# Kernel tuning notes

Hardware: AMD Instinct MI355X
Metric: run time of the kernel (lower is better)

Reference implementation:

```python
import jax, jax.numpy as jnp
import numpy as np

N_NODES = 50000
IN_CH = 128
HID = 256
N_EDGES = 500000


def setup_inputs() -> dict:
    key = jax.random.key(0)
    ks = jax.random.split(key, 16)
    glorot = lambda k, fi, fo: jax.random.normal(k, (fi, fo), jnp.float32) * (2.0 / (fi + fo)) ** 0.5
    return {
        "x": jax.random.normal(ks[0], (N_NODES, IN_CH), jnp.float32),
        "edge_index": jax.random.randint(ks[1], (2, N_EDGES), 0, N_NODES),
        "guidance_features": jax.random.normal(ks[2], (N_NODES, IN_CH), jnp.float32),
        "labels": jax.random.randint(ks[3], (N_NODES,), 0, 2),
        # state_encoder: Linear(3*in, hid) -> ReLU -> Linear(hid, hid)
        "se_w1": glorot(ks[4], IN_CH * 3, HID), "se_b1": jnp.zeros((HID,), jnp.float32),
        "se_w2": glorot(ks[5], HID, HID), "se_b2": jnp.zeros((HID,), jnp.float32),
        # policy_net: Linear(hid, hid//2) -> ReLU -> Linear(hid//2, 1) -> Sigmoid
        "pw1": glorot(ks[6], HID, HID // 2), "pb1": jnp.zeros((HID // 2,), jnp.float32),
        "pw2": glorot(ks[7], HID // 2, 1), "pb2": jnp.zeros((1,), jnp.float32),
        # value_predictor: Linear(hid, hid//2) -> ReLU -> Linear(hid//2, 1)
        "vw1": glorot(ks[8], HID, HID // 2), "vb1": jnp.zeros((HID // 2,), jnp.float32),
        "vw2": glorot(ks[9], HID // 2, 1), "vb2": jnp.zeros((1,), jnp.float32),
    }


def reference(x, edge_index, guidance_features, labels,
              se_w1, se_b1, se_w2, se_b2,
              pw1, pb1, pw2, pb2,
              vw1, vb1, vw2, vb2):
    row, col = edge_index[0], edge_index[1]
    # gather + concat -> [E, 3*in_ch]
    state = jnp.concatenate([x[row], x[col], guidance_features[col]], axis=1)
    # state_encoder
    h = jax.nn.relu(state @ se_w1 + se_b1) @ se_w2 + se_b2  # [E, hid]
    # policy_net (sigmoid)
    probs = jax.nn.sigmoid(jax.nn.relu(h @ pw1 + pb1) @ pw2 + pb2)  # [E, 1]
    # eval-mode actions (training=False branch)
    actions = (probs > 0.5).astype(jnp.float32)  # [E, 1]
    # value predictor + BCE-with-logits vs labels[row]
    z = jax.nn.relu(h @ vw1 + vb1) @ vw2 + vb2  # [E, 1]
    y = labels[row].astype(jnp.float32)[:, None]
    value_loss = jnp.mean(jnp.maximum(z, 0.0) - z * y + jnp.log1p(jnp.exp(-jnp.abs(z))))
    # NOTE: torch version also returns edge_index[:, actions>0] which has a
    # data-dependent shape; we return the dense action mask instead (jit-safe).
    return value_loss, actions
```

## Files before the change

### kernel.cpp

```cpp
#include <hip/hip_runtime.h>
#include <cstddef>

#define TE 56
#define NTHREADS 512

typedef float v2f __attribute__((ext_vector_type(2)));

#define PK_LO(accv, av, wv) \
  asm("v_pk_fma_f32 %0, %1, %2, %0 op_sel:[0,0,0] op_sel_hi:[0,1,1]" \
      : "+v"(accv) : "v"(av), "v"(wv))
#define PK_HI(accv, av, wv) \
  asm("v_pk_fma_f32 %0, %1, %2, %0 op_sel:[1,0,0] op_sel_hi:[1,1,1]" \
      : "+v"(accv) : "v"(av), "v"(wv))

#define SH_OFF    0
#define SW_OFF    14336
#define SW2_OFF   (SW_OFF + 4096)
#define SLOSS_OFF (SW2_OFF + 256)
#define SROW_OFF  (SLOSS_OFF + 64)
#define SCOL_OFF  (SROW_OFF + 64)
#define SMEM_FLOATS (SCOL_OFF + 64)

__device__ __forceinline__ void gld16(const float* g, float* l) {
  __builtin_amdgcn_global_load_lds(
      (const __attribute__((address_space(1))) void*)g,
      (__attribute__((address_space(3))) void*)l, 16, 0, 0);
}

__global__ __launch_bounds__(NTHREADS, 4)
void fused_edge_mlp(
    const float* __restrict__ x,
    const int*   __restrict__ edge_index,
    const float* __restrict__ gf,
    const int*   __restrict__ labels,
    const float* __restrict__ se_w1, const float* __restrict__ se_b1,
    const float* __restrict__ se_w2, const float* __restrict__ se_b2,
    const float* __restrict__ pw1,  const float* __restrict__ pb1,
    const float* __restrict__ pw2,  const float* __restrict__ pb2,
    const float* __restrict__ vw1,  const float* __restrict__ vb1,
    const float* __restrict__ vw2,  const float* __restrict__ vb2,
    float* __restrict__ out,
    float* __restrict__ ws_partial,
    int n_edges)
{
  extern __shared__ float smem[];
  float* sH    = smem + SH_OFF;
  float* sA    = smem + SH_OFF;
  float* sW    = smem + SW_OFF;
  float* sW2   = smem + SW2_OFF;
  float* sLoss = smem + SLOSS_OFF;
  int*   sRow  = (int*)(smem + SROW_OFF);
  int*   sCol  = (int*)(smem + SCOL_OFF);

  const int t  = threadIdx.x;
  const int e0 = blockIdx.x * TE;

  const int tc  = t & 31;
  const int teh = t >> 5;
  const int te  = teh & 7;
  const int ch  = teh >> 3;
  const int colBase = ch * 128 + tc * 4;

  const int wr  = t >> 6;
  const int wc4 = t & 63;

  if (t < TE) {
    int eg = e0 + t;
    sRow[t] = (eg < n_edges) ? edge_index[eg] : 0;
  } else if (t < 2 * TE) {
    int eg = e0 + (t - TE);
    sCol[t - TE] = (eg < n_edges) ? edge_index[(size_t)n_edges + eg] : 0;
  } else if (t >= 128 && t < 384) {
    int c = t - 128;
    sW2[c] = (c < 128) ? pw2[c] : vw2[c - 128];
  }

  v2f acc[7][2];
  auto zero_acc = [&]() {
    #pragma unroll
    for (int i = 0; i < 7; ++i) {
      acc[i][0] = v2f{0.f, 0.f};
      acc[i][1] = v2f{0.f, 0.f};
    }
  };

  auto issueW1 = [&](int c, int b) {
    gld16(&se_w1[((size_t)(c * 8 + wr)) * 256 + wc4 * 4], &sW[b * 2048 + t * 4]);
  };
  auto issueW2 = [&](int c, int b) {
    gld16(&se_w2[((size_t)(c * 8 + wr)) * 256 + wc4 * 4], &sW[b * 2048 + t * 4]);
  };
  auto issueW3 = [&](int c, int b) {
    int row = c * 8 + wr;
    const float* src = (wc4 < 32) ? &pw1[(size_t)row * 128 + wc4 * 4]
                                  : &vw1[(size_t)row * 128 + (wc4 - 32) * 4];
    gld16(src, &sW[b * 2048 + t * 4]);
  };

  auto stageA_issue = [&](int seg, int b) {
    const float* src = (seg == 2) ? gf : x;
    const int*   idx = (seg == 0) ? sRow : sCol;
    float* dst = sA + b * 7168;
    #pragma unroll
    for (int j = 0; j < 3; ++j) {
      int i4 = t + j * NTHREADS;
      int r = i4 >> 5, c4 = i4 & 31;
      gld16(&src[(size_t)idx[r] * 128 + c4 * 4], &dst[i4 * 4]);
    }
    if (t < 256) {
      int i4 = t + 3 * NTHREADS;
      int r = i4 >> 5, c4 = i4 & 31;
      gld16(&src[(size_t)idx[r] * 128 + c4 * 4], &dst[i4 * 4]);
    }
  };

  auto gemmC = [&](const float* Ak, const int LDA, const float* Wb) {
    #pragma unroll
    for (int k4 = 0; k4 < 2; ++k4) {
      v2f w[4][2];
      #pragma unroll
      for (int dk = 0; dk < 4; ++dk) {
        float4 wv = *(const float4*)&Wb[(k4 * 4 + dk) * 256 + colBase];
        w[dk][0] = v2f{wv.x, wv.y};
        w[dk][1] = v2f{wv.z, wv.w};
      }
      #pragma unroll
      for (int i = 0; i < 7; ++i) {
        float4 av = *(const float4*)&Ak[(te * 7 + i) * LDA + k4 * 4];
        v2f pa01 = v2f{av.x, av.y};
        v2f pa23 = v2f{av.z, av.w};
        PK_LO(acc[i][0], pa01, w[0][0]);
        PK_LO(acc[i][1], pa01, w[0][1]);
        PK_HI(acc[i][0], pa01, w[1][0]);
        PK_HI(acc[i][1], pa01, w[1][1]);
        PK_LO(acc[i][0], pa23, w[2][0]);
        PK_LO(acc[i][1], pa23, w[2][1]);
        PK_HI(acc[i][0], pa23, w[3][0]);
        PK_HI(acc[i][1], pa23, w[3][1]);
      }
    }
  };

  issueW1(0, 0);
  __syncthreads();
  stageA_issue(0, 0);
  __syncthreads();

  zero_acc();

  for (int seg = 0; seg < 3; ++seg) {
    const float* Ab = sA + (seg & 1) * 7168;
    if (seg < 2) stageA_issue(seg + 1, (seg + 1) & 1);
    #pragma unroll 4
    for (int kc = 0; kc < 16; ++kc) {
      int c = seg * 16 + kc;
      if (c < 47) issueW1(c + 1, (c + 1) & 1);
      else        issueW2(0, 0);
      gemmC(Ab + kc * 8, 128, sW + (c & 1) * 2048);
      __syncthreads();
    }
  }

  {
    float4 b = *(const float4*)&se_b1[colBase];
    #pragma unroll
    for (int i = 0; i < 7; ++i) {
      float4 hv;
      hv.x = fmaxf(acc[i][0].x + b.x, 0.f);
      hv.y = fmaxf(acc[i][0].y + b.y, 0.f);
      hv.z = fmaxf(acc[i][1].x + b.z, 0.f);
      hv.w = fmaxf(acc[i][1].y + b.w, 0.f);
      *(float4*)&sH[(te * 7 + i) * 256 + colBase] = hv;
    }
    zero_acc();
  }
  __syncthreads();

  #pragma unroll 4
  for (int c = 0; c < 32; ++c) {
    if (c < 31) issueW2(c + 1, (c + 1) & 1);
    else        issueW3(0, 0);
    gemmC(sH + c * 8, 256, sW + (c & 1) * 2048);
    __syncthreads();
  }

  {
    float4 b = *(const float4*)&se_b2[colBase];
    #pragma unroll
    for (int i = 0; i < 7; ++i) {
      float4 hv;
      hv.x = acc[i][0].x + b.x;
      hv.y = acc[i][0].y + b.y;
      hv.z = acc[i][1].x + b.z;
      hv.w = acc[i][1].y + b.w;
      *(float4*)&sH[(te * 7 + i) * 256 + colBase] = hv;
    }
    zero_acc();
  }
  __syncthreads();

  #pragma unroll 4
  for (int c = 0; c < 32; ++c) {
    if (c < 31) issueW3(c + 1, (c + 1) & 1);
    gemmC(sH + c * 8, 256, sW + (c & 1) * 2048);
    __syncthreads();
  }

  {
    float4 b = (ch == 0) ? *(const float4*)&pb1[tc * 4] : *(const float4*)&vb1[tc * 4];
    #pragma unroll
    for (int i = 0; i < 7; ++i) {
      float4 hv;
      hv.x = fmaxf(acc[i][0].x + b.x, 0.f);
      hv.y = fmaxf(acc[i][0].y + b.y, 0.f);
      hv.z = fmaxf(acc[i][1].x + b.z, 0.f);
      hv.w = fmaxf(acc[i][1].y + b.w, 0.f);
      *(float4*)&sH[(te * 7 + i) * 256 + colBase] = hv;
    }
  }
  __syncthreads();

  if (t < 4 * 2 * TE) {
    int lk   = t & 3;
    int d    = t >> 2;
    int head = (d >= TE);
    int edge = d - head * TE;
    int base = head * 128 + lk * 32;
    float p = 0.f;
    #pragma unroll
    for (int kk = 0; kk < 32; kk += 4) {
      float4 r4 = *(const float4*)&sH[edge * 256 + base + kk];
      float4 w4 = *(const float4*)&sW2[base + kk];
      p = fmaf(r4.x, w4.x, p);
      p = fmaf(r4.y, w4.y, p);
      p = fmaf(r4.z, w4.z, p);
      p = fmaf(r4.w, w4.w, p);
    }
    p += __shfl_xor(p, 1);
    p += __shfl_xor(p, 2);
    if (lk == 0) {
      int eg = e0 + edge;
      bool valid = eg < n_edges;
      if (head == 0) {
        float logit = p + pb2[0];
        if (valid) out[1 + eg] = (logit > 0.f) ? 1.f : 0.f;
      } else {
        float term = 0.f;
        if (valid) {
          float z = p + vb2[0];
          float yv = (float)labels[sRow[edge]];
          term = fmaxf(z, 0.f) - z * yv + log1pf(expf(-fabsf(z)));
        }
        sLoss[edge] = term;
      }
    }
  }
  __syncthreads();
  if (t == 0) {
    float s = 0.f;
    #pragma unroll 4
    for (int i = 0; i < TE; ++i) s += sLoss[i];
    ws_partial[blockIdx.x] = s;
  }
}

__global__ void finalize_loss(const float* __restrict__ ws, float* __restrict__ out,
                              int n, double invE)
{
  __shared__ double sd[256];
  double a = 0.0;
  for (int i = threadIdx.x; i < n; i += 256) a += (double)ws[i];
  sd[threadIdx.x] = a;
  __syncthreads();
  for (int off = 128; off > 0; off >>= 1) {
    if ((int)threadIdx.x < off) sd[threadIdx.x] += sd[threadIdx.x + off];
    __syncthreads();
  }
  if (threadIdx.x == 0) out[0] = (float)(sd[0] * invE);
}

extern "C" void kernel_launch(void* const* d_in, const int* in_sizes, int n_in,
                              void* d_out, int out_size, void* d_ws, size_t ws_size,
                              hipStream_t stream) {
  const float* x      = (const float*)d_in[0];
  const int*   ei     = (const int*)  d_in[1];
  const float* gf     = (const float*)d_in[2];
  const int*   labels = (const int*)  d_in[3];
  const float* se_w1  = (const float*)d_in[4];
  const float* se_b1  = (const float*)d_in[5];
  const float* se_w2  = (const float*)d_in[6];
  const float* se_b2  = (const float*)d_in[7];
  const float* pw1    = (const float*)d_in[8];
  const float* pb1    = (const float*)d_in[9];
  const float* pw2    = (const float*)d_in[10];
  const float* pb2    = (const float*)d_in[11];
  const float* vw1    = (const float*)d_in[12];
  const float* vb1    = (const float*)d_in[13];
  const float* vw2    = (const float*)d_in[14];
  const float* vb2    = (const float*)d_in[15];

  int n_edges = in_sizes[1] / 2;
  int nblocks = (n_edges + TE - 1) / TE;
  float* out = (float*)d_out;
  float* ws  = (float*)d_ws;

  size_t shmem = SMEM_FLOATS * sizeof(float);
  (void)hipFuncSetAttribute((const void*)fused_edge_mlp,
                            hipFuncAttributeMaxDynamicSharedMemorySize, (int)shmem);

  fused_edge_mlp<<<dim3(nblocks), dim3(NTHREADS), shmem, stream>>>(
      x, ei, gf, labels,
      se_w1, se_b1, se_w2, se_b2,
      pw1, pb1, pw2, pb2,
      vw1, vb1, vw2, vb2,
      out, ws, n_edges);

  finalize_loss<<<dim3(1), dim3(256), 0, stream>>>(ws, out, nblocks, 1.0 / (double)n_edges);
}
```

Baseline: 2.596 ms.

## Raise edge tile to 64 and load gather indices directly from global memory

```diff
diff --git a/kernel.cpp b/kernel.cpp
--- a/kernel.cpp
+++ b/kernel.cpp
@@ -1,7 +1,7 @@
 #include <hip/hip_runtime.h>
 #include <cstddef>
 
-#define TE 56
+#define TE 64
 #define NTHREADS 512
 
 typedef float v2f __attribute__((ext_vector_type(2)));
@@ -13,13 +13,8 @@
   asm("v_pk_fma_f32 %0, %1, %2, %0 op_sel:[1,0,0] op_sel_hi:[1,1,1]" \
       : "+v"(accv) : "v"(av), "v"(wv))
 
-#define SH_OFF    0
-#define SW_OFF    14336
-#define SW2_OFF   (SW_OFF + 4096)
-#define SLOSS_OFF (SW2_OFF + 256)
-#define SROW_OFF  (SLOSS_OFF + 64)
-#define SCOL_OFF  (SROW_OFF + 64)
-#define SMEM_FLOATS (SCOL_OFF + 64)
+#define SW_OFF 16384
+#define SMEM_FLOATS 20480
 
 __device__ __forceinline__ void gld16(const float* g, float* l) {
   __builtin_amdgcn_global_load_lds(
@@ -44,13 +39,10 @@
     int n_edges)
 {
   extern __shared__ float smem[];
-  float* sH    = smem + SH_OFF;
-  float* sA    = smem + SH_OFF;
+  float* sH    = smem;
+  float* sA    = smem;
   float* sW    = smem + SW_OFF;
-  float* sW2   = smem + SW2_OFF;
-  float* sLoss = smem + SLOSS_OFF;
-  int*   sRow  = (int*)(smem + SROW_OFF);
-  int*   sCol  = (int*)(smem + SCOL_OFF);
+  float* sLoss = smem + SW_OFF;
 
   const int t  = threadIdx.x;
   const int e0 = blockIdx.x * TE;
@@ -64,21 +56,10 @@
   const int wr  = t >> 6;
   const int wc4 = t & 63;
 
-  if (t < TE) {
-    int eg = e0 + t;
-    sRow[t] = (eg < n_edges) ? edge_index[eg] : 0;
-  } else if (t < 2 * TE) {
-    int eg = e0 + (t - TE);
-    sCol[t - TE] = (eg < n_edges) ? edge_index[(size_t)n_edges + eg] : 0;
-  } else if (t >= 128 && t < 384) {
-    int c = t - 128;
-    sW2[c] = (c < 128) ? pw2[c] : vw2[c - 128];
-  }
-
-  v2f acc[7][2];
+  v2f acc[8][2];
   auto zero_acc = [&]() {
     #pragma unroll
-    for (int i = 0; i < 7; ++i) {
+    for (int i = 0; i < 8; ++i) {
       acc[i][0] = v2f{0.f, 0.f};
       acc[i][1] = v2f{0.f, 0.f};
     }
@@ -98,19 +79,18 @@
   };
 
   auto stageA_issue = [&](int seg, int b) {
-    const float* src = (seg == 2) ? gf : x;
-    const int*   idx = (seg == 0) ? sRow : sCol;
-    float* dst = sA + b * 7168;
-    #pragma unroll
-    for (int j = 0; j < 3; ++j) {
-      int i4 = t + j * NTHREADS;
-      int r = i4 >> 5, c4 = i4 & 31;
-      gld16(&src[(size_t)idx[r] * 128 + c4 * 4], &dst[i4 * 4]);
-    }
-    if (t < 256) {
-      int i4 = t + 3 * NTHREADS;
-      int r = i4 >> 5, c4 = i4 & 31;
-      gld16(&src[(size_t)idx[r] * 128 + c4 * 4], &dst[i4 * 4]);
+    float* dst = sA + b * 8192;
+    #pragma unroll
+    for (int j = 0; j < 4; ++j) {
+      int r  = (t >> 5) + j * 16;
+      int eg = e0 + r;
+      bool v = eg < n_edges;
+      int node;
+      const float* src;
+      if (seg == 0)      { node = v ? edge_index[eg] : 0;                   src = x;  }
+      else if (seg == 1) { node = v ? edge_index[(size_t)n_edges + eg] : 0; src = x;  }
+      else               { node = v ? edge_index[(size_t)n_edges + eg] : 0; src = gf; }
+      gld16(&src[(size_t)node * 128 + tc * 4], &dst[(t + j * 512) * 4]);
     }
   };
 
@@ -125,8 +105,8 @@
         w[dk][1] = v2f{wv.z, wv.w};
       }
       #pragma unroll
-      for (int i = 0; i < 7; ++i) {
-        float4 av = *(const float4*)&Ak[(te * 7 + i) * LDA + k4 * 4];
+      for (int i = 0; i < 8; ++i) {
+        float4 av = *(const float4*)&Ak[(te * 8 + i) * LDA + k4 * 4];
         v2f pa01 = v2f{av.x, av.y};
         v2f pa23 = v2f{av.z, av.w};
         PK_LO(acc[i][0], pa01, w[0][0]);
@@ -142,14 +122,13 @@
   };
 
   issueW1(0, 0);
-  __syncthreads();
   stageA_issue(0, 0);
   __syncthreads();
 
   zero_acc();
 
   for (int seg = 0; seg < 3; ++seg) {
-    const float* Ab = sA + (seg & 1) * 7168;
+    const float* Ab = sA + (seg & 1) * 8192;
     if (seg < 2) stageA_issue(seg + 1, (seg + 1) & 1);
     #pragma unroll 4
     for (int kc = 0; kc < 16; ++kc) {
@@ -164,13 +143,13 @@
   {
     float4 b = *(const float4*)&se_b1[colBase];
     #pragma unroll
-    for (int i = 0; i < 7; ++i) {
+    for (int i = 0; i < 8; ++i) {
       float4 hv;
       hv.x = fmaxf(acc[i][0].x + b.x, 0.f);
       hv.y = fmaxf(acc[i][0].y + b.y, 0.f);
       hv.z = fmaxf(acc[i][1].x + b.z, 0.f);
       hv.w = fmaxf(acc[i][1].y + b.w, 0.f);
-      *(float4*)&sH[(te * 7 + i) * 256 + colBase] = hv;
+      *(float4*)&sH[(te * 8 + i) * 256 + colBase] = hv;
     }
     zero_acc();
   }
@@ -187,13 +166,13 @@
   {
     float4 b = *(const float4*)&se_b2[colBase];
     #pragma unroll
-    for (int i = 0; i < 7; ++i) {
+    for (int i = 0; i < 8; ++i) {
       float4 hv;
       hv.x = acc[i][0].x + b.x;
       hv.y = acc[i][0].y + b.y;
       hv.z = acc[i][1].x + b.z;
       hv.w = acc[i][1].y + b.w;
-      *(float4*)&sH[(te * 7 + i) * 256 + colBase] = hv;
+      *(float4*)&sH[(te * 8 + i) * 256 + colBase] = hv;
     }
     zero_acc();
   }
@@ -209,28 +188,28 @@
   {
     float4 b = (ch == 0) ? *(const float4*)&pb1[tc * 4] : *(const float4*)&vb1[tc * 4];
     #pragma unroll
-    for (int i = 0; i < 7; ++i) {
+    for (int i = 0; i < 8; ++i) {
       float4 hv;
       hv.x = fmaxf(acc[i][0].x + b.x, 0.f);
       hv.y = fmaxf(acc[i][0].y + b.y, 0.f);
       hv.z = fmaxf(acc[i][1].x + b.z, 0.f);
       hv.w = fmaxf(acc[i][1].y + b.w, 0.f);
-      *(float4*)&sH[(te * 7 + i) * 256 + colBase] = hv;
-    }
-  }
-  __syncthreads();
-
-  if (t < 4 * 2 * TE) {
+      *(float4*)&sH[(te * 8 + i) * 256 + colBase] = hv;
+    }
+  }
+  __syncthreads();
+
+  {
     int lk   = t & 3;
     int d    = t >> 2;
-    int head = (d >= TE);
-    int edge = d - head * TE;
-    int base = head * 128 + lk * 32;
+    int head = d >> 6;
+    int edge = d & 63;
+    const float* w2 = head ? vw2 : pw2;
     float p = 0.f;
     #pragma unroll
     for (int kk = 0; kk < 32; kk += 4) {
-      float4 r4 = *(const float4*)&sH[edge * 256 + base + kk];
-      float4 w4 = *(const float4*)&sW2[base + kk];
+      float4 r4 = *(const float4*)&sH[edge * 256 + head * 128 + lk * 32 + kk];
+      float4 w4 = *(const float4*)&w2[lk * 32 + kk];
       p = fmaf(r4.x, w4.x, p);
       p = fmaf(r4.y, w4.y, p);
       p = fmaf(r4.z, w4.z, p);
@@ -248,7 +227,8 @@
         float term = 0.f;
         if (valid) {
           float z = p + vb2[0];
-          float yv = (float)labels[sRow[edge]];
+          int srcn = edge_index[eg];
+          float yv = (float)labels[srcn];
           term = fmaxf(z, 0.f) - z * yv + log1pf(expf(-fabsf(z)));
         }
         sLoss[edge] = term;
```

After: 2.540 ms. -2.2%, faster.
